# Kernel tuning notes

Measured on AMD Instinct MI355X. Metric: run time of the kernel, lower is better.

## Reference

```python
import jax, jax.numpy as jnp
import numpy as np

T, B, I, H = 512, 64, 512, 512

def setup_inputs() -> dict:
    key = jax.random.key(0)
    ks = jax.random.split(key, 16)
    s_i = 1.0 / np.sqrt(I)
    s_h = 1.0 / np.sqrt(H)
    return {
        "input": jax.random.normal(ks[0], (T, B, I), jnp.float32),
        "hidden": jax.random.normal(ks[1], (B, H), jnp.float32),
        "zt_w_w": jax.random.uniform(ks[2], (1, I), jnp.float32, -s_i, s_i),
        "zt_w_b": jax.random.uniform(ks[3], (1,), jnp.float32, -s_i, s_i),
        "zt_u_w": jax.random.uniform(ks[4], (1, H), jnp.float32, -s_h, s_h),
        "zt_u_b": jax.random.uniform(ks[5], (1,), jnp.float32, -s_h, s_h),
        "rt_w_w": jax.random.uniform(ks[6], (1, I), jnp.float32, -s_i, s_i),
        "rt_w_b": jax.random.uniform(ks[7], (1,), jnp.float32, -s_i, s_i),
        "rt_u_w": jax.random.uniform(ks[8], (1, H), jnp.float32, -s_h, s_h),
        "rt_u_b": jax.random.uniform(ks[9], (1,), jnp.float32, -s_h, s_h),
        "h_w_w": jax.random.uniform(ks[10], (H, I), jnp.float32, -s_i, s_i),
        "h_w_b": jax.random.uniform(ks[11], (H,), jnp.float32, -s_i, s_i),
        "h_u_w": jax.random.uniform(ks[12], (H, H), jnp.float32, -s_h, s_h),
        "h_u_b": jax.random.uniform(ks[13], (H,), jnp.float32, -s_h, s_h),
    }

def reference(input, hidden, zt_w_w, zt_w_b, zt_u_w, zt_u_b,
              rt_w_w, rt_w_b, rt_u_w, rt_u_b, h_w_w, h_w_b, h_u_w, h_u_b):
    # Input-dependent projections are h-independent: precompute over all T.
    xz = jnp.einsum('tbi,oi->tbo', input, zt_w_w) + zt_w_b  # [T,B,1]
    xr = jnp.einsum('tbi,oi->tbo', input, rt_w_w) + rt_w_b  # [T,B,1]
    xn = jnp.einsum('tbi,hi->tbh', input, h_w_w) + h_w_b    # [T,B,H]

    def step(h, xs):
        xz_t, xr_t, xn_t = xs
        zt = jax.nn.sigmoid(xz_t + h @ zt_u_w.T + zt_u_b)   # [B,1]
        rt = jax.nn.sigmoid(xr_t + h @ rt_u_w.T + rt_u_b)   # [B,1]
        # NOTE: faithful to source: h_u(hidden) * rt (gate applied AFTER linear)
        nt = jnp.tanh(xn_t + (h @ h_u_w.T + h_u_b) * rt)    # [B,H]
        h_new = (1.0 - zt) * nt + zt * h
        return h_new, h_new

    hidden_final, output = jax.lax.scan(step, hidden, (xz, xr, xn))
    return output, hidden_final
```

## Files before the change

kernel.cpp:

```cpp
#include <hip/hip_runtime.h>
#include <hip/hip_fp16.h>

#define T_DIM 512
#define B_DIM 64
#define I_DIM 512
#define H_DIM 512
#define BH (B_DIM * H_DIM)
#define TBH ((size_t)T_DIM * BH)

typedef __attribute__((ext_vector_type(8))) short short8;
typedef __attribute__((ext_vector_type(4))) float f32x4;

#define SW16(r, k) ((r) * 512 + ((k) ^ (((r) & 15) << 3)))

__device__ __forceinline__ unsigned short f2bf(float x) {
    unsigned int u = __float_as_uint(x);
    u = u + 0x7FFFu + ((u >> 16) & 1u);
    return (unsigned short)(u >> 16);
}
__device__ __forceinline__ float bf2f(unsigned short s) {
    return __uint_as_float(((unsigned int)s) << 16);
}
__device__ __forceinline__ float uasf(unsigned int u) { return __uint_as_float(u); }

__device__ __forceinline__ void ld128_coh(uint4& d, const void* p) {
    asm volatile("global_load_dwordx4 %0, %1, off sc0 sc1"
                 : "=v"(d) : "v"(p) : "memory");
}
__device__ __forceinline__ void ld128_coh_wait(uint4& d, const void* p) {
    asm volatile("global_load_dwordx4 %0, %1, off sc0 sc1\n\t"
                 "s_waitcnt vmcnt(0)"
                 : "=v"(d) : "v"(p) : "memory");
}
__device__ __forceinline__ void ld32f(float& d, const void* p) {
    asm volatile("global_load_dword %0, %1, off" : "=v"(d) : "v"(p));
}
__device__ __forceinline__ void ld32u(unsigned int& d, const void* p) {
    asm volatile("global_load_dword %0, %1, off" : "=v"(d) : "v"(p));
}

__global__ __launch_bounds__(256) void xzr_kernel(
    const float* __restrict__ input,
    const float* __restrict__ zw, const float* __restrict__ zb,
    const float* __restrict__ rw, const float* __restrict__ rb,
    unsigned int* __restrict__ xzr, unsigned int* __restrict__ flags)
{
    const int tid = threadIdx.x, bx = blockIdx.x;
    if (bx == 0 && tid < 32) flags[tid] = 0u;
    const int row = bx * 4 + (tid >> 6);
    const int lane = tid & 63;
    const float* p = input + (size_t)row * I_DIM + lane * 8;
    float x[8], z[8], r[8];
    *(float4*)(x)     = *(const float4*)(p);
    *(float4*)(x + 4) = *(const float4*)(p + 4);
    *(float4*)(z)     = *(const float4*)(zw + lane * 8);
    *(float4*)(z + 4) = *(const float4*)(zw + lane * 8 + 4);
    *(float4*)(r)     = *(const float4*)(rw + lane * 8);
    *(float4*)(r + 4) = *(const float4*)(rw + lane * 8 + 4);
    float pz = 0.f, pr = 0.f;
#pragma unroll
    for (int i = 0; i < 8; i++) { pz += x[i] * z[i]; pr += x[i] * r[i]; }
#pragma unroll
    for (int off = 32; off > 0; off >>= 1) {
        pz += __shfl_xor(pz, off);
        pr += __shfl_xor(pr, off);
    }
    if (lane == 0) {
        unsigned int uz = __half_as_ushort(__float2half(pz + zb[0]));
        unsigned int ur = __half_as_ushort(__float2half(pr + rb[0]));
        xzr[row] = (uz << 16) | ur;
    }
}

#define APITCH 40

__global__ __launch_bounds__(256, 2) void xn_gemm_kernel(
    const float* __restrict__ A, const float* __restrict__ W,
    const float* __restrict__ bias, float* __restrict__ C)
{
    __shared__ __align__(16) unsigned short a_hi[64 * APITCH], a_lo[64 * APITCH];
    __shared__ __align__(16) unsigned short b_hi[64 * APITCH], b_lo[64 * APITCH];
    const int tid = threadIdx.x;
    const int bx = blockIdx.x;
    const int mt = bx >> 3, ntile = bx & 7;
    const int wv = tid >> 6, lane = tid & 63;
    const int srow = tid >> 2, skseg = (tid & 3) * 8;
    const int m = lane & 15;
    const int ko = (lane >> 4) * 8;

    f32x4 ahh[4], ahl[4], alh[4];
#pragma unroll
    for (int i = 0; i < 4; i++) { ahh[i] = (f32x4)0.f; ahl[i] = (f32x4)0.f; alh[i] = (f32x4)0.f; }

    for (int kt = 0; kt < 16; ++kt) {
        {
            float fa[8], fb[8];
            const float* pa = A + (size_t)(mt * 64 + srow) * I_DIM + kt * 32 + skseg;
            *(float4*)(fa)     = *(const float4*)(pa);
            *(float4*)(fa + 4) = *(const float4*)(pa + 4);
            const float* pb = W + (size_t)(ntile * 64 + srow) * I_DIM + kt * 32 + skseg;
            *(float4*)(fb)     = *(const float4*)(pb);
            *(float4*)(fb + 4) = *(const float4*)(pb + 4);
            short8 hi, lo;
#pragma unroll
            for (int i = 0; i < 8; i++) {
                unsigned short h = f2bf(fa[i]);
                hi[i] = (short)h; lo[i] = (short)f2bf(fa[i] - bf2f(h));
            }
            *(short8*)&a_hi[srow * APITCH + skseg] = hi;
            *(short8*)&a_lo[srow * APITCH + skseg] = lo;
#pragma unroll
            for (int i = 0; i < 8; i++) {
                unsigned short h = f2bf(fb[i]);
                hi[i] = (short)h; lo[i] = (short)f2bf(fb[i] - bf2f(h));
            }
            *(short8*)&b_hi[srow * APITCH + skseg] = hi;
            *(short8*)&b_lo[srow * APITCH + skseg] = lo;
        }
        __syncthreads();
        short8 vah = *(const short8*)&a_hi[(wv * 16 + m) * APITCH + ko];
        short8 val = *(const short8*)&a_lo[(wv * 16 + m) * APITCH + ko];
#pragma unroll
        for (int ns = 0; ns < 4; ++ns) {
            short8 vbh = *(const short8*)&b_hi[(ns * 16 + m) * APITCH + ko];
            short8 vbl = *(const short8*)&b_lo[(ns * 16 + m) * APITCH + ko];
            ahh[ns] = __builtin_amdgcn_mfma_f32_16x16x32_bf16(vah, vbh, ahh[ns], 0, 0, 0);
            ahl[ns] = __builtin_amdgcn_mfma_f32_16x16x32_bf16(vah, vbl, ahl[ns], 0, 0, 0);
            alh[ns] = __builtin_amdgcn_mfma_f32_16x16x32_bf16(val, vbh, alh[ns], 0, 0, 0);
        }
        __syncthreads();
    }
#pragma unroll
    for (int ns = 0; ns < 4; ++ns) {
#pragma unroll
        for (int rr = 0; rr < 4; ++rr) {
            int rowd = wv * 16 + (lane >> 4) * 4 + rr;
            int cold = ntile * 64 + ns * 16 + (lane & 15);
            float v = ahh[ns][rr] + ahl[ns][rr] + alh[ns][rr] + bias[cold];
            C[(size_t)(mt * 64 + rowd) * H_DIM + cold] = v;
        }
    }
}

__global__ __launch_bounds__(256, 1) void rnn_kernel(
    const float* __restrict__ h0,
    const unsigned int* __restrict__ xzr,
    const float* __restrict__ zuw, const float* __restrict__ ruw,
    const float* __restrict__ zub, const float* __restrict__ rub,
    const float* __restrict__ huw, const float* __restrict__ hub,
    float* __restrict__ out,
    char* __restrict__ xbuf, unsigned int* __restrict__ flags)
{
    __shared__ __align__(16) unsigned short hs_hi[16 * 512], hs_lo[16 * 512];
    __shared__ float zu[512], ru[512];
    __shared__ float zg[16], rg[16];

    const int tid = threadIdx.x;
    const int bid = blockIdx.x;
    const int g = bid >> 3, js = bid & 7;
    const int wv = tid >> 6, lane = tid & 63;
    const int quad = lane >> 4, am = lane & 15;
    const int col = js * 64 + wv * 16 + am;
    const int ko = quad * 8;
    const int gr = tid >> 4, gs = tid & 15;

    for (int i = tid; i < 512; i += 256) { zu[i] = zuw[i]; ru[i] = ruw[i]; }
    const float zbias = zub[0], rbias = rub[0];
    const float hubl = hub[col];

    short8 wh[16], wl[16];
#pragma unroll
    for (int kt = 0; kt < 16; ++kt) {
        float f[8];
        const float* p = huw + (size_t)col * H_DIM + kt * 32 + ko;
        *(float4*)(f)     = *(const float4*)(p);
        *(float4*)(f + 4) = *(const float4*)(p + 4);
#pragma unroll
        for (int i = 0; i < 8; i++) {
            unsigned short h = f2bf(f[i]);
            wh[kt][i] = (short)h;
            wl[kt][i] = (short)f2bf(f[i] - bf2f(h));
        }
    }

#pragma unroll
    for (int i = 0; i < 8; i++) {
        int idx = tid * 4 + i * 1024;
        int row = idx >> 9, k = idx & 511;
        float4 f = *(const float4*)(h0 + (size_t)(g * 16 + row) * H_DIM + k);
        float fa[4] = {f.x, f.y, f.z, f.w};
        unsigned int h_[4], l_[4];
#pragma unroll
        for (int j = 0; j < 4; j++) {
            h_[j] = f2bf(fa[j]);
            l_[j] = f2bf(fa[j] - bf2f((unsigned short)h_[j]));
        }
        int a = SW16(row, k);
        uint2 hv = { h_[0] | (h_[1] << 16), h_[2] | (h_[3] << 16) };
        uint2 lv = { l_[0] | (l_[1] << 16), l_[2] | (l_[3] << 16) };
        *(uint2*)&hs_hi[a] = hv;
        *(uint2*)&hs_lo[a] = lv;
    }
    float hkeep[4];
#pragma unroll
    for (int rr = 0; rr < 4; ++rr)
        hkeep[rr] = h0[(size_t)(g * 16 + quad * 4 + rr) * H_DIM + col];
    __syncthreads();

    float xnv0, xnv1, xnv2, xnv3;
    unsigned int zrw;
#define PREFETCH(tt) do {                                                     \
        const float* xp_ = out + (size_t)(tt) * BH +                          \
                           (size_t)(g * 16 + quad * 4) * H_DIM + col;         \
        ld32f(xnv0, xp_);        ld32f(xnv1, xp_ + H_DIM);                    \
        ld32f(xnv2, xp_ + 2 * H_DIM); ld32f(xnv3, xp_ + 3 * H_DIM);           \
        ld32u(zrw, xzr + (tt) * B_DIM + g * 16 + gr);                         \
    } while (0)
    PREFETCH(0);

    for (int t = 0; t < T_DIM; ++t) {
        asm volatile("s_waitcnt vmcnt(0)"
                     : "+v"(xnv0), "+v"(xnv1), "+v"(xnv2), "+v"(xnv3), "+v"(zrw)
                     :: "memory");
        float pz = 0.f, pr = 0.f;
#pragma unroll
        for (int i = 0; i < 8; i++) {
            int k = gs * 4 + i * 64;
            int a = SW16(gr, k);
            uint2 hw = *(const uint2*)&hs_hi[a];
            uint2 lw = *(const uint2*)&hs_lo[a];
            float4 zv = *(const float4*)&zu[k];
            float4 rv = *(const float4*)&ru[k];
            float h0f = uasf(hw.x << 16) + uasf(lw.x << 16);
            float h1f = uasf(hw.x & 0xFFFF0000u) + uasf(lw.x & 0xFFFF0000u);
            float h2f = uasf(hw.y << 16) + uasf(lw.y << 16);
            float h3f = uasf(hw.y & 0xFFFF0000u) + uasf(lw.y & 0xFFFF0000u);
            pz += h0f * zv.x + h1f * zv.y + h2f * zv.z + h3f * zv.w;
            pr += h0f * rv.x + h1f * rv.y + h2f * rv.z + h3f * rv.w;
        }
#pragma unroll
        for (int off = 8; off > 0; off >>= 1) {
            pz += __shfl_xor(pz, off);
            pr += __shfl_xor(pr, off);
        }
        if (gs == 0) {
            float xzf = __half2float(__ushort_as_half((unsigned short)(zrw >> 16)));
            float xrf = __half2float(__ushort_as_half((unsigned short)(zrw & 0xFFFFu)));
            zg[gr] = 1.f / (1.f + __expf(-(xzf + pz + zbias)));
            rg[gr] = 1.f / (1.f + __expf(-(xrf + pr + rbias)));
        }
        __syncthreads();

        f32x4 hh = (f32x4)0.f, hl = (f32x4)0.f, lh = (f32x4)0.f;
#pragma unroll
        for (int kt = 0; kt < 16; ++kt) {
            short8 ah = *(const short8*)&hs_hi[SW16(am, kt * 32 + ko)];
            short8 al = *(const short8*)&hs_lo[SW16(am, kt * 32 + ko)];
            hh = __builtin_amdgcn_mfma_f32_16x16x32_bf16(ah, wh[kt], hh, 0, 0, 0);
            hl = __builtin_amdgcn_mfma_f32_16x16x32_bf16(ah, wl[kt], hl, 0, 0, 0);
            lh = __builtin_amdgcn_mfma_f32_16x16x32_bf16(al, wh[kt], lh, 0, 0, 0);
        }

        float xn_a[4] = {xnv0, xnv1, xnv2, xnv3};
        float* op = out + (size_t)t * BH;
        char* xb = xbuf + ((size_t)(((t & 1) * 4) + g)) * 32768;
        unsigned short* bhp = (unsigned short*)xb;
        unsigned short* blp = (unsigned short*)(xb + 16384);
#pragma unroll
        for (int rr = 0; rr < 4; ++rr) {
            int rl = quad * 4 + rr;
            float gemm = hh[rr] + hl[rr] + lh[rr] + hubl;
            float x2 = xn_a[rr] + gemm * rg[rl];
            x2 = fminf(fmaxf(x2, -30.f), 30.f);
            float e = __expf(2.f * x2);
            float ntv = (e - 1.f) / (e + 1.f);
            float hv = (1.f - zg[rl]) * ntv + zg[rl] * hkeep[rr];
            op[(size_t)(g * 16 + rl) * H_DIM + col] = hv;
            unsigned short hu = f2bf(hv);
            unsigned short lu = f2bf(hv - bf2f(hu));
            __hip_atomic_store(&bhp[rl * 512 + col], hu, __ATOMIC_RELAXED, __HIP_MEMORY_SCOPE_AGENT);
            __hip_atomic_store(&blp[rl * 512 + col], lu, __ATOMIC_RELAXED, __HIP_MEMORY_SCOPE_AGENT);
            hkeep[rr] = hv;
        }
        asm volatile("s_waitcnt vmcnt(0)" ::: "memory");
        __syncthreads();
        if (tid == 0)
            __hip_atomic_store(&flags[g * 8 + js], (unsigned int)(t + 1),
                               __ATOMIC_RELAXED, __HIP_MEMORY_SCOPE_AGENT);
        if (t == T_DIM - 1) break;

        PREFETCH(t + 1);

        if (lane < 8) {
            const unsigned int* fp = flags + g * 8 + lane;
            while (__hip_atomic_load(fp, __ATOMIC_RELAXED, __HIP_MEMORY_SCOPE_AGENT)
                   < (unsigned int)(t + 1))
                __builtin_amdgcn_s_sleep(1);
        }

        const char* src = xbuf + ((size_t)(((t & 1) * 4) + g)) * 32768 + tid * 16;
        uint4 v[8];
#pragma unroll
        for (int i = 0; i < 7; i++) ld128_coh(v[i], src + i * 4096);
        ld128_coh_wait(v[7], src + 7 * 4096);
#pragma unroll
        for (int i = 0; i < 8; i++) {
            int usidx = tid * 8 + (i & 3) * 2048;
            int row = usidx >> 9, ku = usidx & 511;
            unsigned short* dst = (i < 4) ? hs_hi : hs_lo;
            *(uint4*)&dst[SW16(row, ku)] = v[i];
        }
        __syncthreads();
    }

#pragma unroll
    for (int rr = 0; rr < 4; ++rr)
        out[TBH + (size_t)(g * 16 + quad * 4 + rr) * H_DIM + col] = hkeep[rr];
#undef PREFETCH
}

extern "C" void kernel_launch(void* const* d_in, const int* in_sizes, int n_in,
                              void* d_out, int out_size, void* d_ws, size_t ws_size,
                              hipStream_t stream)
{
    const float* input  = (const float*)d_in[0];
    const float* hidden = (const float*)d_in[1];
    const float* zt_w_w = (const float*)d_in[2];
    const float* zt_w_b = (const float*)d_in[3];
    const float* zt_u_w = (const float*)d_in[4];
    const float* zt_u_b = (const float*)d_in[5];
    const float* rt_w_w = (const float*)d_in[6];
    const float* rt_w_b = (const float*)d_in[7];
    const float* rt_u_w = (const float*)d_in[8];
    const float* rt_u_b = (const float*)d_in[9];
    const float* h_w_w  = (const float*)d_in[10];
    const float* h_w_b  = (const float*)d_in[11];
    const float* h_u_w  = (const float*)d_in[12];
    const float* h_u_b  = (const float*)d_in[13];
    float* out = (float*)d_out;

    unsigned int* flags = (unsigned int*)d_ws;
    char* xbuf = (char*)d_ws + 4096;
    unsigned int* xzr = (unsigned int*)((char*)d_ws + 4096 + 262144);

    xzr_kernel<<<dim3(8192), dim3(256), 0, stream>>>(input, zt_w_w, zt_w_b,
                                                     rt_w_w, rt_w_b, xzr, flags);
    xn_gemm_kernel<<<dim3(4096), dim3(256), 0, stream>>>(input, h_w_w, h_w_b, out);
    rnn_kernel<<<dim3(32), dim3(256), 0, stream>>>(hidden, xzr, zt_u_w, rt_u_w,
                                                   zt_u_b, rt_u_b, h_u_w, h_u_b,
                                                   out, xbuf, flags);
}
```

Before: 2.374 ms.

## Replace flag-based inter-block sync with parity-tagged hidden-state exchange

Drops the per-step flag store and spin-wait between the 8 blocks of each batch group. Each hidden value's bf16 hi/lo halves now carry a parity tag in their low bit, so readers poll the exchange buffer until every element shows the expected tag. Values are staged in LDS and written as coherent 128-bit chunks, and one barrier moves past the MFMA loop. This removes a flag round-trip per step but drops one mantissa bit from each half. Correctness depends on the 4-step tag cycle and on the double-buffered exchange never being overwritten before it is read.

```diff
diff --git a/kernel.cpp b/kernel.cpp
--- a/kernel.cpp
+++ b/kernel.cpp
@@ -18,8 +18,8 @@
     u = u + 0x7FFFu + ((u >> 16) & 1u);
     return (unsigned short)(u >> 16);
 }
-__device__ __forceinline__ float bf2f(unsigned short s) {
-    return __uint_as_float(((unsigned int)s) << 16);
+__device__ __forceinline__ float bf2f(unsigned int s) {
+    return __uint_as_float(s << 16);
 }
 __device__ __forceinline__ float uasf(unsigned int u) { return __uint_as_float(u); }
 
@@ -32,6 +32,13 @@
                  "s_waitcnt vmcnt(0)"
                  : "=v"(d) : "v"(p) : "memory");
 }
+__device__ __forceinline__ void st128_coh(void* p, uint4 v) {
+    asm volatile("global_store_dword %0, %1, off sc0 sc1\n\t"
+                 "global_store_dword %0, %2, off offset:4 sc0 sc1\n\t"
+                 "global_store_dword %0, %3, off offset:8 sc0 sc1\n\t"
+                 "global_store_dword %0, %4, off offset:12 sc0 sc1"
+                 :: "v"(p), "v"(v.x), "v"(v.y), "v"(v.z), "v"(v.w) : "memory");
+}
 __device__ __forceinline__ void ld32f(float& d, const void* p) {
     asm volatile("global_load_dword %0, %1, off" : "=v"(d) : "v"(p));
 }
@@ -43,10 +50,9 @@
     const float* __restrict__ input,
     const float* __restrict__ zw, const float* __restrict__ zb,
     const float* __restrict__ rw, const float* __restrict__ rb,
-    unsigned int* __restrict__ xzr, unsigned int* __restrict__ flags)
+    unsigned int* __restrict__ xzr)
 {
     const int tid = threadIdx.x, bx = blockIdx.x;
-    if (bx == 0 && tid < 32) flags[tid] = 0u;
     const int row = bx * 4 + (tid >> 6);
     const int lane = tid & 63;
     const float* p = input + (size_t)row * I_DIM + lane * 8;
@@ -148,12 +154,13 @@
     const float* __restrict__ zuw, const float* __restrict__ ruw,
     const float* __restrict__ zub, const float* __restrict__ rub,
     const float* __restrict__ huw, const float* __restrict__ hub,
-    float* __restrict__ out,
-    char* __restrict__ xbuf, unsigned int* __restrict__ flags)
+    float* __restrict__ out, unsigned int* __restrict__ xch)
 {
     __shared__ __align__(16) unsigned short hs_hi[16 * 512], hs_lo[16 * 512];
     __shared__ float zu[512], ru[512];
     __shared__ float zg[16], rg[16];
+    __shared__ __align__(16) unsigned int stage[16 * 68];
+    __shared__ int wgbad;
 
     const int tid = threadIdx.x;
     const int bid = blockIdx.x;
@@ -193,7 +200,7 @@
 #pragma unroll
         for (int j = 0; j < 4; j++) {
             h_[j] = f2bf(fa[j]);
-            l_[j] = f2bf(fa[j] - bf2f((unsigned short)h_[j]));
+            l_[j] = f2bf(fa[j] - bf2f(h_[j]));
         }
         int a = SW16(row, k);
         uint2 hv = { h_[0] | (h_[1] << 16), h_[2] | (h_[3] << 16) };
@@ -249,7 +256,6 @@
             zg[gr] = 1.f / (1.f + __expf(-(xzf + pz + zbias)));
             rg[gr] = 1.f / (1.f + __expf(-(xrf + pr + rbias)));
         }
-        __syncthreads();
 
         f32x4 hh = (f32x4)0.f, hl = (f32x4)0.f, lh = (f32x4)0.f;
 #pragma unroll
@@ -260,12 +266,12 @@
             hl = __builtin_amdgcn_mfma_f32_16x16x32_bf16(ah, wl[kt], hl, 0, 0, 0);
             lh = __builtin_amdgcn_mfma_f32_16x16x32_bf16(al, wh[kt], lh, 0, 0, 0);
         }
-
+        __syncthreads();
+
+        const unsigned int tau = (unsigned int)((t + 1) & 3);
+        const unsigned int hb = (tau >> 1) & 1u, lb = tau & 1u;
         float xn_a[4] = {xnv0, xnv1, xnv2, xnv3};
         float* op = out + (size_t)t * BH;
-        char* xb = xbuf + ((size_t)(((t & 1) * 4) + g)) * 32768;
-        unsigned short* bhp = (unsigned short*)xb;
-        unsigned short* blp = (unsigned short*)(xb + 16384);
 #pragma unroll
         for (int rr = 0; rr < 4; ++rr) {
             int rl = quad * 4 + rr;
@@ -276,41 +282,62 @@
             float ntv = (e - 1.f) / (e + 1.f);
             float hv = (1.f - zg[rl]) * ntv + zg[rl] * hkeep[rr];
             op[(size_t)(g * 16 + rl) * H_DIM + col] = hv;
-            unsigned short hu = f2bf(hv);
-            unsigned short lu = f2bf(hv - bf2f(hu));
-            __hip_atomic_store(&bhp[rl * 512 + col], hu, __ATOMIC_RELAXED, __HIP_MEMORY_SCOPE_AGENT);
-            __hip_atomic_store(&blp[rl * 512 + col], lu, __ATOMIC_RELAXED, __HIP_MEMORY_SCOPE_AGENT);
+            unsigned int hu = ((unsigned int)f2bf(hv) & 0xFFFEu) | hb;
+            float rem = hv - bf2f(hu);
+            unsigned int lu = ((unsigned int)f2bf(rem) & 0xFFFEu) | lb;
+            stage[rl * 68 + wv * 16 + am] = (hu << 16) | lu;
             hkeep[rr] = hv;
         }
-        asm volatile("s_waitcnt vmcnt(0)" ::: "memory");
+        if (t == T_DIM - 1) break;
         __syncthreads();
-        if (tid == 0)
-            __hip_atomic_store(&flags[g * 8 + js], (unsigned int)(t + 1),
-                               __ATOMIC_RELAXED, __HIP_MEMORY_SCOPE_AGENT);
-        if (t == T_DIM - 1) break;
-
+
+        unsigned int* xchp = xch + ((size_t)((t & 1) * 4 + g)) * 8192;
+        {
+            uint4 val = *(const uint4*)&stage[(tid >> 4) * 68 + (tid & 15) * 4];
+            st128_coh(xchp + (tid >> 4) * 512 + js * 64 + (tid & 15) * 4, val);
+        }
         PREFETCH(t + 1);
-
-        if (lane < 8) {
-            const unsigned int* fp = flags + g * 8 + lane;
-            while (__hip_atomic_load(fp, __ATOMIC_RELAXED, __HIP_MEMORY_SCOPE_AGENT)
-                   < (unsigned int)(t + 1))
-                __builtin_amdgcn_s_sleep(1);
-        }
-
-        const char* src = xbuf + ((size_t)(((t & 1) * 4) + g)) * 32768 + tid * 16;
-        uint4 v[8];
-#pragma unroll
-        for (int i = 0; i < 7; i++) ld128_coh(v[i], src + i * 4096);
-        ld128_coh_wait(v[7], src + 7 * 4096);
-#pragma unroll
-        for (int i = 0; i < 8; i++) {
-            int usidx = tid * 8 + (i & 3) * 2048;
-            int row = usidx >> 9, ku = usidx & 511;
-            unsigned short* dst = (i < 4) ? hs_hi : hs_lo;
-            *(uint4*)&dst[SW16(row, ku)] = v[i];
-        }
-        __syncthreads();
+        __builtin_amdgcn_s_sleep(6);
+
+        const char* src = (const char*)xchp;
+        for (;;) {
+            if (tid == 0) wgbad = 0;
+            uint4 v[8];
+#pragma unroll
+            for (int i = 0; i < 7; i++)
+                ld128_coh(v[i], src + (size_t)(tid + i * 256) * 16);
+            ld128_coh_wait(v[7], src + (size_t)(tid + 7 * 256) * 16);
+#pragma unroll
+            for (int i = 0; i < 8; i++) {
+                int c = tid + i * 256;
+                int row = c >> 7, kcol = (c & 127) * 4;
+                unsigned int hi01 = __builtin_amdgcn_perm(v[i].y, v[i].x, 0x07060302u);
+                unsigned int hi23 = __builtin_amdgcn_perm(v[i].w, v[i].z, 0x07060302u);
+                unsigned int lo01 = __builtin_amdgcn_perm(v[i].y, v[i].x, 0x05040100u);
+                unsigned int lo23 = __builtin_amdgcn_perm(v[i].w, v[i].z, 0x05040100u);
+                int a = SW16(row, kcol);
+                uint2 hvv = {hi01, hi23}, lvv = {lo01, lo23};
+                *(uint2*)&hs_hi[a] = hvv;
+                *(uint2*)&hs_lo[a] = lvv;
+            }
+            __syncthreads();
+            const unsigned int ph = hb * 0x00010001u, pl = lb * 0x00010001u;
+            int ok = 1;
+#pragma unroll
+            for (int i = 0; i < 8; i++) {
+                int c = tid + i * 256;
+                int a = SW16(c >> 7, (c & 127) * 4);
+                uint2 hvv = *(const uint2*)&hs_hi[a];
+                uint2 lvv = *(const uint2*)&hs_lo[a];
+                ok &= (((hvv.x ^ ph) & 0x00010001u) == 0u);
+                ok &= (((hvv.y ^ ph) & 0x00010001u) == 0u);
+                ok &= (((lvv.x ^ pl) & 0x00010001u) == 0u);
+                ok &= (((lvv.y ^ pl) & 0x00010001u) == 0u);
+            }
+            if (!ok) wgbad = 1;
+            __syncthreads();
+            if (!wgbad) break;
+        }
     }
 
 #pragma unroll
@@ -339,14 +366,13 @@
     const float* h_u_b  = (const float*)d_in[13];
     float* out = (float*)d_out;
 
-    unsigned int* flags = (unsigned int*)d_ws;
-    char* xbuf = (char*)d_ws + 4096;
-    unsigned int* xzr = (unsigned int*)((char*)d_ws + 4096 + 262144);
+    unsigned int* xch = (unsigned int*)d_ws;
+    unsigned int* xzr = (unsigned int*)((char*)d_ws + 262144);
 
     xzr_kernel<<<dim3(8192), dim3(256), 0, stream>>>(input, zt_w_w, zt_w_b,
-                                                     rt_w_w, rt_w_b, xzr, flags);
+                                                     rt_w_w, rt_w_b, xzr);
     xn_gemm_kernel<<<dim3(4096), dim3(256), 0, stream>>>(input, h_w_w, h_w_b, out);
     rnn_kernel<<<dim3(32), dim3(256), 0, stream>>>(hidden, xzr, zt_u_w, rt_u_w,
                                                    zt_u_b, rt_u_b, h_u_w, h_u_b,
-                                                   out, xbuf, flags);
-}
+                                                   out, xch);
+}
```

Measured after the change: 2.463 ms. 3.8% more time.
